# Performance work log

Hardware: AMD Instinct MI355X
Metric: run time of the kernel (lower is better)

Reference implementation:

```python
import jax, jax.numpy as jnp
import numpy as np

N_NODES = 100000


def _gcn_conv(x, W, b, row, col, norm, n):
    # PyG GCNConv: h = x @ W, then symmetric-normalized scatter-add, then bias
    h = x @ W                          # [N, out]
    msg = h[col] * norm[:, None]       # gather at source nodes, scale per-edge
    out = jax.ops.segment_sum(msg, row, num_segments=n)  # scatter-add to dest
    return out + b


def setup_inputs() -> dict:
    key = jax.random.key(0)
    k1, k2, k3, k4, k5, k6 = jax.random.split(key, 6)
    F_in, H, C = 128, 128, 64
    E = 1600000
    x = jax.random.normal(k1, (N_NODES, F_in), dtype=jnp.float32)
    edge_index = jax.random.randint(k2, (2, E), 0, N_NODES, dtype=jnp.int64)
    s1 = 1.0 / np.sqrt(F_in)
    s2 = 1.0 / np.sqrt(H)
    W1 = jax.random.uniform(k3, (F_in, H), jnp.float32, -s1, s1)
    b1 = jax.random.uniform(k4, (H,), jnp.float32, -s1, s1)
    W2 = jax.random.uniform(k5, (H, C), jnp.float32, -s2, s2)
    b2 = jax.random.uniform(k6, (C,), jnp.float32, -s2, s2)
    return {"x": x, "edge_index": edge_index, "W1": W1, "b1": b1, "W2": W2, "b2": b2}


def reference(x, edge_index, W1, b1, W2, b2):
    n = x.shape[0]
    # add self-loops (GCNConv default)
    loops = jnp.arange(n, dtype=edge_index.dtype)
    row = jnp.concatenate([edge_index[0], loops])  # destination
    col = jnp.concatenate([edge_index[1], loops])  # source
    # symmetric normalization deg^{-1/2}[row] * deg^{-1/2}[col]
    deg = jax.ops.segment_sum(jnp.ones_like(row, dtype=x.dtype), row, num_segments=n)
    dinv = jnp.where(deg > 0, jax.lax.rsqrt(deg), 0.0)
    norm = dinv[row] * dinv[col]       # [E+N]
    h = jax.nn.relu(_gcn_conv(x, W1, b1, row, col, norm, n))
    # dropout is identity in eval mode
    out = _gcn_conv(h, W2, b2, row, col, norm, n)
    return jax.nn.log_softmax(out, axis=1)
```

## Files before the change

kernel.cpp:

```cpp
#include <hip/hip_runtime.h>
#include <hip/hip_fp16.h>
#include <cstdint>
#include <cstddef>

#define TPB 256
#define CAP 64
#define FWSHIFT 9
#define FWROWS 512
#define CAPB 96
#define DEC_ITERS 32


using half8 = __attribute__((ext_vector_type(8))) _Float16;
using f32x4 = __attribute__((ext_vector_type(4))) float;
using i32x4 = __attribute__((ext_vector_type(4))) int;

struct GemmSm {
    _Float16 Wl[32 * 64 * 8];
    _Float16 Of[4][16 * 136];
};
struct FillSm { int cur[FWROWS]; };
union MegaSm { GemmSm g; FillSm f; };

__global__ __launch_bounds__(256)
void k_setup(const void* __restrict__ ei, int E, int N,
             const float* __restrict__ W2, _Float16* __restrict__ wf2,
             int* __restrict__ bpack, int* __restrict__ bcnt,
             int nDec, int nFW) {
    const int b = blockIdx.x;
    const int tid = threadIdx.x;

    if (b < 8) {
        int i = b * TPB + tid;
        int k  = i >> 4;
        int n0 = (i & 15) * 4;
        float4 w = ((const float4*)W2)[i];
        int ct = n0 >> 4, kb = k >> 5;
        int lane0 = ((k >> 3) & 3) * 16 + (n0 & 15);
        int j = k & 7;
        int base = ((ct * 4 + kb) * 64 + lane0) * 8 + j;
        wf2[base]      = (_Float16)w.x;
        wf2[base + 8]  = (_Float16)w.y;
        wf2[base + 16] = (_Float16)w.z;
        wf2[base + 24] = (_Float16)w.w;
    } else {
        __shared__ int cur[256];
        __shared__ int bad;
        const int dblk = b - 8;
        if (tid == 0) bad = 0;
        for (int f = tid; f < nFW; f += TPB) cur[f] = 0;
        __syncthreads();
        {
            long long v = ((const long long*)ei)[tid];
            if (v < 0 || v >= (long long)N) bad = 1;
        }
        __syncthreads();
        const int is64 = !bad;
        const int base = dblk * (TPB * DEC_ITERS);
        const long long* e64 = (const long long*)ei;
        const int* e32 = (const int*)ei;

        for (int it = 0; it < DEC_ITERS; it += 4) {
            int d[4], s[4]; bool val[4];
#pragma unroll
            for (int k = 0; k < 4; ++k) {
                int e = base + (it + k) * TPB + tid;
                val[k] = e < E;
                if (val[k]) {
                    if (is64) { d[k] = (int)e64[e]; s[k] = (int)e64[(long long)E + e]; }
                    else      { d[k] = e32[e];      s[k] = e32[E + e]; }
                }
            }
#pragma unroll
            for (int k = 0; k < 4; ++k) {
                if (val[k]) {
                    int fw  = d[k] >> FWSHIFT;
                    int pos = atomicAdd(&cur[fw], 1);
                    if (pos < CAPB)
                        bpack[((size_t)fw * nDec + dblk) * CAPB + pos] =
                            ((d[k] & (FWROWS - 1)) << 17) | s[k];
                }
            }
        }
        __syncthreads();
        for (int f = tid; f < nFW; f += TPB) {
            int c = cur[f];
            bcnt[(size_t)f * nDec + dblk] = c > CAPB ? CAPB : c;
        }
    }
}

__global__ __launch_bounds__(256)
void k_mega(const int* __restrict__ bpack, const int* __restrict__ bcnt,
            int nDec, int N,
            int* __restrict__ cnt, float* __restrict__ dinv,
            int* __restrict__ slots,
            const float* __restrict__ x, const float* __restrict__ W1,
            __half* __restrict__ xw1, int nFW, int nGemm) {
    __shared__ __align__(16) MegaSm sm;
    const int tid = threadIdx.x;

    if ((int)blockIdx.x < nFW) {
        const int fw = blockIdx.x;
        const int lo = fw << FWSHIFT;
        for (int i = tid; i < FWROWS; i += TPB) sm.f.cur[i] = 0;
        __syncthreads();

        for (int s = tid; s < nDec; s += TPB) {
            const int c = bcnt[(size_t)fw * nDec + s];
            const int* bp = bpack + ((size_t)fw * nDec + s) * CAPB;
            int j = 0;
            for (; j + 3 < c; j += 4) {
                i32x4 u = __builtin_nontemporal_load((const i32x4*)(bp + j));
                int dl0 = u[0] >> 17, s0 = u[0] & 0x1FFFF;
                int dl1 = u[1] >> 17, s1 = u[1] & 0x1FFFF;
                int dl2 = u[2] >> 17, s2 = u[2] & 0x1FFFF;
                int dl3 = u[3] >> 17, s3 = u[3] & 0x1FFFF;
                int q0 = atomicAdd(&sm.f.cur[dl0], 1);
                int q1 = atomicAdd(&sm.f.cur[dl1], 1);
                int q2 = atomicAdd(&sm.f.cur[dl2], 1);
                int q3 = atomicAdd(&sm.f.cur[dl3], 1);
                if (q0 < CAP) slots[(size_t)(lo + dl0) * CAP + q0] = s0;
                if (q1 < CAP) slots[(size_t)(lo + dl1) * CAP + q1] = s1;
                if (q2 < CAP) slots[(size_t)(lo + dl2) * CAP + q2] = s2;
                if (q3 < CAP) slots[(size_t)(lo + dl3) * CAP + q3] = s3;
            }
            for (; j < c; ++j) {
                int v = __builtin_nontemporal_load(bp + j);
                int dl = v >> 17, sv = v & 0x1FFFF;
                int pos = atomicAdd(&sm.f.cur[dl], 1);
                if (pos < CAP) slots[(size_t)(lo + dl) * CAP + pos] = sv;
            }
        }
        __syncthreads();
        for (int i = tid; i < FWROWS; i += TPB) {
            int node = lo + i;
            if (node < N) {
                int cc = sm.f.cur[i];
                cnt[node]  = cc;
                dinv[node] = rsqrtf((float)cc + 1.0f);
            }
        }
    } else {
        const int gb = (int)blockIdx.x - nFW;
        for (int i = tid; i < 4096; i += TPB) {
            float4 w = ((const float4*)W1)[i];
            int k  = i >> 5;
            int n0 = (i & 31) * 4;
            int ct = n0 >> 4, kb = k >> 5;
            int lane0 = ((k >> 3) & 3) * 16 + (n0 & 15);
            int j = k & 7;
            int bs = ((ct * 4 + kb) * 64 + lane0) * 8 + j;
            sm.g.Wl[bs]      = (_Float16)w.x;
            sm.g.Wl[bs + 8]  = (_Float16)w.y;
            sm.g.Wl[bs + 16] = (_Float16)w.z;
            sm.g.Wl[bs + 24] = (_Float16)w.w;
        }
        __syncthreads();
        const half8* wl = (const half8*)sm.g.Wl;
        const int wave = tid >> 6, lane = tid & 63;
        const int m = lane & 15, quad = lane >> 4;
        const int nRowTiles = (N + 15) >> 4;

        for (int rt = gb * 4 + wave; rt < nRowTiles; rt += nGemm * 4) {
            const int row0 = rt * 16;
            const int arow = row0 + m;
            const bool rvalid = arow < N;
            const float* xrow = x + (size_t)(rvalid ? arow : 0) * 128;

            f32x4 acc[8];
#pragma unroll
            for (int ct = 0; ct < 8; ++ct) acc[ct] = (f32x4){0.f, 0.f, 0.f, 0.f};

#pragma unroll
            for (int kb = 0; kb < 4; ++kb) {
                const float4* ap = (const float4*)(xrow + kb * 32 + quad * 8);
                float4 a0 = ap[0], a1 = ap[1];
                half8 a;
                a[0] = (_Float16)a0.x; a[1] = (_Float16)a0.y;
                a[2] = (_Float16)a0.z; a[3] = (_Float16)a0.w;
                a[4] = (_Float16)a1.x; a[5] = (_Float16)a1.y;
                a[6] = (_Float16)a1.z; a[7] = (_Float16)a1.w;
#pragma unroll
                for (int ct = 0; ct < 8; ++ct) {
                    half8 bfr = wl[(ct * 4 + kb) * 64 + lane];
                    acc[ct] = __builtin_amdgcn_mfma_f32_16x16x32_f16(a, bfr, acc[ct], 0, 0, 0);
                }
            }

            _Float16* myO = &sm.g.Of[wave][0];
#pragma unroll
            for (int ct = 0; ct < 8; ++ct)
#pragma unroll
                for (int r = 0; r < 4; ++r)
                    myO[(quad * 4 + r) * 136 + ct * 16 + m] = (_Float16)acc[ct][r];
            int vr = N - row0; if (vr > 16) vr = 16;
            float4* dst = (float4*)(xw1 + (size_t)row0 * 128);
            for (int i = lane; i < vr * 16; i += 64) {
                int r = i >> 4, q = i & 15;
                dst[r * 16 + q] = *(const float4*)&myO[r * 136 + q * 8];
            }
        }
    }
}

__global__ __launch_bounds__(256)
void k_g1g2(const __half* __restrict__ xw1, const int* __restrict__ cnt,
            const float* __restrict__ dinv,
            const int* __restrict__ slots, const float* __restrict__ bias,
            const half8* __restrict__ wf2, __half* __restrict__ xw2, int N) {
    __shared__ __align__(16) _Float16 Ht[16 * 136];
    __shared__ __align__(16) _Float16 Of[16 * 72];
    __shared__ float dv16[16];

    const int row0 = blockIdx.x * 16;
    const int local = threadIdx.x >> 4;
    const int lane16 = threadIdx.x & 15;
    const int node = row0 + local;

    {
        union { __half2 h2[4]; float4 f; } u;
        float dvn = 0.f;
        if (node < N) {
            int cn = cnt[node];
            int len = cn > CAP ? CAP : cn;
            dvn = dinv[node];
            const int* sl = slots + (size_t)node * CAP;
            float acc[8];
            {
                float4 raw = *(const float4*)(xw1 + (size_t)node * 128 + lane16 * 8);
                const __half2* hp = (const __half2*)&raw;
#pragma unroll
                for (int k = 0; k < 4; ++k) {
                    float2 f = __half22float2(hp[k]);
                    acc[2 * k] = dvn * f.x; acc[2 * k + 1] = dvn * f.y;
                }
            }
            int j = 0;
            for (; j + 3 < len; j += 4) {
                i32x4 cc = __builtin_nontemporal_load((const i32x4*)(sl + j));
                float dv0 = dinv[cc[0]];
                float dv1 = dinv[cc[1]];
                float dv2 = dinv[cc[2]];
                float dv3 = dinv[cc[3]];
                float4 raw0 = *(const float4*)(xw1 + (size_t)cc[0] * 128 + lane16 * 8);
                float4 raw1 = *(const float4*)(xw1 + (size_t)cc[1] * 128 + lane16 * 8);
                float4 raw2 = *(const float4*)(xw1 + (size_t)cc[2] * 128 + lane16 * 8);
                float4 raw3 = *(const float4*)(xw1 + (size_t)cc[3] * 128 + lane16 * 8);
                const __half2* h0 = (const __half2*)&raw0;
                const __half2* h1 = (const __half2*)&raw1;
                const __half2* h2 = (const __half2*)&raw2;
                const __half2* h3 = (const __half2*)&raw3;
#pragma unroll
                for (int k = 0; k < 4; ++k) {
                    float2 f0 = __half22float2(h0[k]);
                    float2 f1 = __half22float2(h1[k]);
                    float2 f2 = __half22float2(h2[k]);
                    float2 f3 = __half22float2(h3[k]);
                    acc[2 * k]     = fmaf(dv0, f0.x, fmaf(dv1, f1.x,
                                     fmaf(dv2, f2.x, fmaf(dv3, f3.x, acc[2 * k]))));
                    acc[2 * k + 1] = fmaf(dv0, f0.y, fmaf(dv1, f1.y,
                                     fmaf(dv2, f2.y, fmaf(dv3, f3.y, acc[2 * k + 1]))));
                }
            }
            for (; j < len; ++j) {
                int c = __builtin_nontemporal_load(sl + j);
                float dv = dinv[c];
                float4 raw = *(const float4*)(xw1 + (size_t)c * 128 + lane16 * 8);
                const __half2* hp = (const __half2*)&raw;
#pragma unroll
                for (int k = 0; k < 4; ++k) {
                    float2 f = __half22float2(hp[k]);
                    acc[2 * k]     = fmaf(dv, f.x, acc[2 * k]);
                    acc[2 * k + 1] = fmaf(dv, f.y, acc[2 * k + 1]);
                }
            }
            float4 b01 = ((const float4*)bias)[lane16 * 2];
            float4 b23 = ((const float4*)bias)[lane16 * 2 + 1];
            float v[8];
            v[0] = b01.x + dvn * acc[0]; v[1] = b01.y + dvn * acc[1];
            v[2] = b01.z + dvn * acc[2]; v[3] = b01.w + dvn * acc[3];
            v[4] = b23.x + dvn * acc[4]; v[5] = b23.y + dvn * acc[5];
            v[6] = b23.z + dvn * acc[6]; v[7] = b23.w + dvn * acc[7];
#pragma unroll
            for (int k = 0; k < 4; ++k)
                u.h2[k] = __floats2half2_rn(fmaxf(v[2 * k], 0.f), fmaxf(v[2 * k + 1], 0.f));
        } else {
            u.f = make_float4(0.f, 0.f, 0.f, 0.f);
        }
        if (lane16 == 0) dv16[local] = dvn;
        *(float4*)(Ht + local * 136 + lane16 * 8) = u.f;
    }
    __syncthreads();

    {
        const int wave = threadIdx.x >> 6, lane = threadIdx.x & 63;
        const int m = lane & 15, quad = lane >> 4;
        f32x4 acc = (f32x4){0.f, 0.f, 0.f, 0.f};
#pragma unroll
        for (int kb = 0; kb < 4; ++kb) {
            half8 a = *(const half8*)(Ht + m * 136 + kb * 32 + quad * 8);
            half8 b = wf2[(wave * 4 + kb) * 64 + lane];
            acc = __builtin_amdgcn_mfma_f32_16x16x32_f16(a, b, acc, 0, 0, 0);
        }
#pragma unroll
        for (int r = 0; r < 4; ++r)
            Of[(quad * 4 + r) * 72 + wave * 16 + m] =
                (_Float16)(acc[r] * dv16[quad * 4 + r]);
    }
    __syncthreads();
    {
        int vr = N - row0; if (vr > 16) vr = 16;
        float4* dst = (float4*)(xw2 + (size_t)row0 * 64);
        for (int i = threadIdx.x; i < vr * 8; i += TPB) {
            int r = i >> 3, q = i & 7;
            dst[r * 8 + q] = *(const float4*)&Of[r * 72 + q * 8];
        }
    }
}

__global__ void k_gather2_lsm(const __half* __restrict__ xws, const int* __restrict__ cnt,
                              const float* __restrict__ dinv,
                              const int* __restrict__ slots,
                              const float* __restrict__ bias, float* __restrict__ out, int N) {
    long long t = (long long)blockIdx.x * TPB + threadIdx.x;
    int node = (int)(t >> 3);
    int lane = (int)(t & 7);
    if (node >= N) return;
    int cn = cnt[node];
    int len = cn > CAP ? CAP : cn;
    float dvn = dinv[node];
    const int* sl = slots + (size_t)node * CAP;
    float a[8];
    {
        float4 raw = *(const float4*)(xws + (size_t)node * 64 + lane * 8);
        const __half2* hp = (const __half2*)&raw;
#pragma unroll
        for (int k = 0; k < 4; ++k) {
            float2 f = __half22float2(hp[k]);
            a[2 * k] = f.x; a[2 * k + 1] = f.y;
        }
    }
    int j = 0;
    for (; j + 3 < len; j += 4) {
        i32x4 cc = __builtin_nontemporal_load((const i32x4*)(sl + j));
        float4 r0 = *(const float4*)(xws + (size_t)cc[0] * 64 + lane * 8);
        float4 r1 = *(const float4*)(xws + (size_t)cc[1] * 64 + lane * 8);
        float4 r2 = *(const float4*)(xws + (size_t)cc[2] * 64 + lane * 8);
        float4 r3 = *(const float4*)(xws + (size_t)cc[3] * 64 + lane * 8);
        const __half2* h0 = (const __half2*)&r0;
        const __half2* h1 = (const __half2*)&r1;
        const __half2* h2 = (const __half2*)&r2;
        const __half2* h3 = (const __half2*)&r3;
#pragma unroll
        for (int k = 0; k < 4; ++k) {
            float2 f0 = __half22float2(h0[k]);
            float2 f1 = __half22float2(h1[k]);
            float2 f2 = __half22float2(h2[k]);
            float2 f3 = __half22float2(h3[k]);
            a[2 * k]     += (f0.x + f1.x) + (f2.x + f3.x);
            a[2 * k + 1] += (f0.y + f1.y) + (f2.y + f3.y);
        }
    }
    for (; j < len; ++j) {
        int c = __builtin_nontemporal_load(sl + j);
        float4 raw = *(const float4*)(xws + (size_t)c * 64 + lane * 8);
        const __half2* hp = (const __half2*)&raw;
#pragma unroll
        for (int k = 0; k < 4; ++k) {
            float2 f = __half22float2(hp[k]);
            a[2 * k] += f.x; a[2 * k + 1] += f.y;
        }
    }
    float4 b01 = ((const float4*)bias)[lane * 2];
    float4 b23 = ((const float4*)bias)[lane * 2 + 1];
    float v[8];
    v[0] = b01.x + dvn * a[0]; v[1] = b01.y + dvn * a[1];
    v[2] = b01.z + dvn * a[2]; v[3] = b01.w + dvn * a[3];
    v[4] = b23.x + dvn * a[4]; v[5] = b23.y + dvn * a[5];
    v[6] = b23.z + dvn * a[6]; v[7] = b23.w + dvn * a[7];

    float m = v[0];
#pragma unroll
    for (int k = 1; k < 8; ++k) m = fmaxf(m, v[k]);
#pragma unroll
    for (int off = 1; off < 8; off <<= 1) m = fmaxf(m, __shfl_xor(m, off));
    float s = 0.f;
#pragma unroll
    for (int k = 0; k < 8; ++k) s += expf(v[k] - m);
#pragma unroll
    for (int off = 1; off < 8; off <<= 1) s += __shfl_xor(s, off);
    float ls = m + logf(s);
    float4 o0 = make_float4(v[0] - ls, v[1] - ls, v[2] - ls, v[3] - ls);
    float4 o1 = make_float4(v[4] - ls, v[5] - ls, v[6] - ls, v[7] - ls);
    ((float4*)(out + (size_t)node * 64))[lane * 2]     = o0;
    ((float4*)(out + (size_t)node * 64))[lane * 2 + 1] = o1;
}

extern "C" void kernel_launch(void* const* d_in, const int* in_sizes, int n_in,
                              void* d_out, int out_size, void* d_ws, size_t ws_size,
                              hipStream_t stream) {
    const float* x  = (const float*)d_in[0];
    const void*  ei = d_in[1];
    const float* W1 = (const float*)d_in[2];
    const float* b1 = (const float*)d_in[3];
    const float* W2 = (const float*)d_in[4];
    const float* b2 = (const float*)d_in[5];
    float* out = (float*)d_out;

    const int N = in_sizes[0] / 128;
    const int E = in_sizes[1] / 2;

    const int nFW  = (N + FWROWS - 1) >> FWSHIFT;
    const int nDec = (E + TPB * DEC_ITERS - 1) / (TPB * DEC_ITERS);
    const int nGemm = 512;

    char* base = (char*)d_ws;
    size_t off = 0;
    auto alloc = [&](size_t bytes) { char* p = base + off; off = (off + bytes + 255) & ~(size_t)255; return p; };
    int*      cnt    = (int*)alloc((size_t)N * sizeof(int));
    float*    dinv   = (float*)alloc((size_t)N * sizeof(float));
    _Float16* wf2    = (_Float16*)alloc(128 * 64 * sizeof(_Float16));
    int*      bcnt   = (int*)alloc((size_t)nFW * nDec * sizeof(int));
    int*      bpack  = (int*)alloc((size_t)nFW * nDec * CAPB * sizeof(int));
    int*      slots  = (int*)alloc((size_t)N * CAP * sizeof(int));
    __half*   xw1    = (__half*)alloc((size_t)N * 128 * sizeof(__half));
    __half*   xw2    = (__half*)alloc((size_t)N * 64 * sizeof(__half));
    (void)ws_size;

    const int nodeTiles = (N + 15) / 16;

    k_setup<<<8 + nDec, TPB, 0, stream>>>(ei, E, N, W2, wf2, bpack, bcnt,
                                          nDec, nFW);

    k_mega<<<nFW + nGemm, TPB, 0, stream>>>(bpack, bcnt, nDec, N, cnt, dinv,
                                            slots, x, W1, xw1, nFW, nGemm);

    k_g1g2<<<nodeTiles, TPB, 0, stream>>>(xw1, cnt, dinv, slots, b1,
                                          (const half8*)wf2, xw2, N);

    {
        long long t = (long long)N * 8;
        k_gather2_lsm<<<(int)((t + TPB - 1) / TPB), TPB, 0, stream>>>(xw2, cnt, dinv, slots, b2, out, N);
    }
}
```

Measured before the change: 260.1 us.

## Stage edge bins in shared memory via prefix scan and write compactly

The edge-decode kernel now counts edges per destination window, runs a shared-memory prefix scan, and scatters the packed edges into a shared buffer. It then writes them contiguously per decode block with per-window base offsets and counts, replacing fixed CAPB-sized per-window slots. This drops the capacity-truncation path and replaces scattered global writes with coalesced ones, shrinking the bpack workspace. The consumer reads with scalar loads at unaligned offsets, and nontemporal loads are replaced by plain loads in all gather kernels. Costs are more syncs and register/LDS pressure in setup, and scalar rather than vector bin reads in k_mega.

Result: faster. 238.2 us (-8.4%).

```diff
diff --git a/kernel.cpp b/kernel.cpp
--- a/kernel.cpp
+++ b/kernel.cpp
@@ -7,13 +7,12 @@
 #define CAP 64
 #define FWSHIFT 9
 #define FWROWS 512
-#define CAPB 96
 #define DEC_ITERS 32
+#define DEC_EDGES (TPB * DEC_ITERS)
 
 
 using half8 = __attribute__((ext_vector_type(8))) _Float16;
 using f32x4 = __attribute__((ext_vector_type(4))) float;
-using i32x4 = __attribute__((ext_vector_type(4))) int;
 
 struct GemmSm {
     _Float16 Wl[32 * 64 * 8];
@@ -25,8 +24,13 @@
 __global__ __launch_bounds__(256)
 void k_setup(const void* __restrict__ ei, int E, int N,
              const float* __restrict__ W2, _Float16* __restrict__ wf2,
-             int* __restrict__ bpack, int* __restrict__ bcnt,
-             int nDec, int nFW) {
+             int* __restrict__ bpack, int* __restrict__ bbase,
+             int* __restrict__ bcnt, int nDec, int nFW) {
+    __shared__ int buf[DEC_EDGES];
+    __shared__ int lcnt[256];
+    __shared__ int lofs[256];
+    __shared__ int sc[256];
+    __shared__ int bad;
     const int b = blockIdx.x;
     const int tid = threadIdx.x;
 
@@ -43,56 +47,73 @@
         wf2[base + 8]  = (_Float16)w.y;
         wf2[base + 16] = (_Float16)w.z;
         wf2[base + 24] = (_Float16)w.w;
-    } else {
-        __shared__ int cur[256];
-        __shared__ int bad;
-        const int dblk = b - 8;
-        if (tid == 0) bad = 0;
-        for (int f = tid; f < nFW; f += TPB) cur[f] = 0;
+        return;
+    }
+
+    const int dblk = b - 8;
+    if (tid == 0) bad = 0;
+    lcnt[tid] = 0;
+    __syncthreads();
+    {
+        long long v = ((const long long*)ei)[tid];
+        if (v < 0 || v >= (long long)N) bad = 1;
+    }
+    __syncthreads();
+    const int is64 = !bad;
+    const int base = dblk * DEC_EDGES;
+    const long long* e64 = (const long long*)ei;
+    const int* e32 = (const int*)ei;
+
+    int pv[DEC_ITERS];
+    int pfw[DEC_ITERS];
+#pragma unroll
+    for (int k = 0; k < DEC_ITERS; ++k) {
+        int e = base + k * TPB + tid;
+        pfw[k] = -1;
+        pv[k] = 0;
+        if (e < E) {
+            int d, s;
+            if (is64) { d = (int)e64[e]; s = (int)e64[(long long)E + e]; }
+            else      { d = e32[e];      s = e32[E + e]; }
+            pfw[k] = d >> FWSHIFT;
+            pv[k]  = ((d & (FWROWS - 1)) << 17) | s;
+            atomicAdd(&lcnt[pfw[k]], 1);
+        }
+    }
+    __syncthreads();
+
+    int c = lcnt[tid];
+    sc[tid] = c;
+    __syncthreads();
+    for (int off = 1; off < 256; off <<= 1) {
+        int v = (tid >= off) ? sc[tid - off] : 0;
         __syncthreads();
-        {
-            long long v = ((const long long*)ei)[tid];
-            if (v < 0 || v >= (long long)N) bad = 1;
-        }
+        sc[tid] += v;
         __syncthreads();
-        const int is64 = !bad;
-        const int base = dblk * (TPB * DEC_ITERS);
-        const long long* e64 = (const long long*)ei;
-        const int* e32 = (const int*)ei;
-
-        for (int it = 0; it < DEC_ITERS; it += 4) {
-            int d[4], s[4]; bool val[4];
-#pragma unroll
-            for (int k = 0; k < 4; ++k) {
-                int e = base + (it + k) * TPB + tid;
-                val[k] = e < E;
-                if (val[k]) {
-                    if (is64) { d[k] = (int)e64[e]; s[k] = (int)e64[(long long)E + e]; }
-                    else      { d[k] = e32[e];      s[k] = e32[E + e]; }
-                }
-            }
-#pragma unroll
-            for (int k = 0; k < 4; ++k) {
-                if (val[k]) {
-                    int fw  = d[k] >> FWSHIFT;
-                    int pos = atomicAdd(&cur[fw], 1);
-                    if (pos < CAPB)
-                        bpack[((size_t)fw * nDec + dblk) * CAPB + pos] =
-                            ((d[k] & (FWROWS - 1)) << 17) | s[k];
-                }
-            }
-        }
-        __syncthreads();
-        for (int f = tid; f < nFW; f += TPB) {
-            int c = cur[f];
-            bcnt[(size_t)f * nDec + dblk] = c > CAPB ? CAPB : c;
-        }
+    }
+    lofs[tid] = sc[tid] - c;
+    __syncthreads();
+#pragma unroll
+    for (int k = 0; k < DEC_ITERS; ++k) {
+        if (pfw[k] >= 0) {
+            int pos = atomicAdd(&lofs[pfw[k]], 1);
+            buf[pos] = pv[k];
+        }
+    }
+    __syncthreads();
+
+    const int total = sc[255];
+    for (int i = tid; i < total; i += TPB)
+        bpack[(size_t)dblk * DEC_EDGES + i] = buf[i];
+    if (tid < nFW) {
+        bbase[(size_t)tid * nDec + dblk] = sc[tid] - c;
+        bcnt [(size_t)tid * nDec + dblk] = c;
     }
 }
 
 __global__ __launch_bounds__(256)
-void k_mega(const int* __restrict__ bpack, const int* __restrict__ bcnt,
-            int nDec, int N,
+void k_mega(const int* __restrict__ bpack, const int* __restrict__ bbase,
+            const int* __restrict__ bcnt, int nDec, int N,
             int* __restrict__ cnt, float* __restrict__ dinv,
             int* __restrict__ slots,
             const float* __restrict__ x, const float* __restrict__ W1,
@@ -107,15 +128,16 @@
         __syncthreads();
 
         for (int s = tid; s < nDec; s += TPB) {
-            const int c = bcnt[(size_t)fw * nDec + s];
-            const int* bp = bpack + ((size_t)fw * nDec + s) * CAPB;
+            const size_t seg = (size_t)fw * nDec + s;
+            const int c = bcnt[seg];
+            const int* bp = bpack + (size_t)s * DEC_EDGES + bbase[seg];
             int j = 0;
             for (; j + 3 < c; j += 4) {
-                i32x4 u = __builtin_nontemporal_load((const i32x4*)(bp + j));
-                int dl0 = u[0] >> 17, s0 = u[0] & 0x1FFFF;
-                int dl1 = u[1] >> 17, s1 = u[1] & 0x1FFFF;
-                int dl2 = u[2] >> 17, s2 = u[2] & 0x1FFFF;
-                int dl3 = u[3] >> 17, s3 = u[3] & 0x1FFFF;
+                int v0 = bp[j], v1 = bp[j + 1], v2 = bp[j + 2], v3 = bp[j + 3];
+                int dl0 = v0 >> 17, s0 = v0 & 0x1FFFF;
+                int dl1 = v1 >> 17, s1 = v1 & 0x1FFFF;
+                int dl2 = v2 >> 17, s2 = v2 & 0x1FFFF;
+                int dl3 = v3 >> 17, s3 = v3 & 0x1FFFF;
                 int q0 = atomicAdd(&sm.f.cur[dl0], 1);
                 int q1 = atomicAdd(&sm.f.cur[dl1], 1);
                 int q2 = atomicAdd(&sm.f.cur[dl2], 1);
@@ -126,7 +148,7 @@
                 if (q3 < CAP) slots[(size_t)(lo + dl3) * CAP + q3] = s3;
             }
             for (; j < c; ++j) {
-                int v = __builtin_nontemporal_load(bp + j);
+                int v = bp[j];
                 int dl = v >> 17, sv = v & 0x1FFFF;
                 int pos = atomicAdd(&sm.f.cur[dl], 1);
                 if (pos < CAP) slots[(size_t)(lo + dl) * CAP + pos] = sv;
@@ -238,15 +260,15 @@
             }
             int j = 0;
             for (; j + 3 < len; j += 4) {
-                i32x4 cc = __builtin_nontemporal_load((const i32x4*)(sl + j));
-                float dv0 = dinv[cc[0]];
-                float dv1 = dinv[cc[1]];
-                float dv2 = dinv[cc[2]];
-                float dv3 = dinv[cc[3]];
-                float4 raw0 = *(const float4*)(xw1 + (size_t)cc[0] * 128 + lane16 * 8);
-                float4 raw1 = *(const float4*)(xw1 + (size_t)cc[1] * 128 + lane16 * 8);
-                float4 raw2 = *(const float4*)(xw1 + (size_t)cc[2] * 128 + lane16 * 8);
-                float4 raw3 = *(const float4*)(xw1 + (size_t)cc[3] * 128 + lane16 * 8);
+                int4 cc = *(const int4*)(sl + j);
+                float dv0 = dinv[cc.x];
+                float dv1 = dinv[cc.y];
+                float dv2 = dinv[cc.z];
+                float dv3 = dinv[cc.w];
+                float4 raw0 = *(const float4*)(xw1 + (size_t)cc.x * 128 + lane16 * 8);
+                float4 raw1 = *(const float4*)(xw1 + (size_t)cc.y * 128 + lane16 * 8);
+                float4 raw2 = *(const float4*)(xw1 + (size_t)cc.z * 128 + lane16 * 8);
+                float4 raw3 = *(const float4*)(xw1 + (size_t)cc.w * 128 + lane16 * 8);
                 const __half2* h0 = (const __half2*)&raw0;
                 const __half2* h1 = (const __half2*)&raw1;
                 const __half2* h2 = (const __half2*)&raw2;
@@ -264,7 +286,7 @@
                 }
             }
             for (; j < len; ++j) {
-                int c = __builtin_nontemporal_load(sl + j);
+                int c = sl[j];
                 float dv = dinv[c];
                 float4 raw = *(const float4*)(xw1 + (size_t)c * 128 + lane16 * 8);
                 const __half2* hp = (const __half2*)&raw;
@@ -343,11 +365,11 @@
     }
     int j = 0;
     for (; j + 3 < len; j += 4) {
-        i32x4 cc = __builtin_nontemporal_load((const i32x4*)(sl + j));
-        float4 r0 = *(const float4*)(xws + (size_t)cc[0] * 64 + lane * 8);
-        float4 r1 = *(const float4*)(xws + (size_t)cc[1] * 64 + lane * 8);
-        float4 r2 = *(const float4*)(xws + (size_t)cc[2] * 64 + lane * 8);
-        float4 r3 = *(const float4*)(xws + (size_t)cc[3] * 64 + lane * 8);
+        int4 cc = *(const int4*)(sl + j);
+        float4 r0 = *(const float4*)(xws + (size_t)cc.x * 64 + lane * 8);
+        float4 r1 = *(const float4*)(xws + (size_t)cc.y * 64 + lane * 8);
+        float4 r2 = *(const float4*)(xws + (size_t)cc.z * 64 + lane * 8);
+        float4 r3 = *(const float4*)(xws + (size_t)cc.w * 64 + lane * 8);
         const __half2* h0 = (const __half2*)&r0;
         const __half2* h1 = (const __half2*)&r1;
         const __half2* h2 = (const __half2*)&r2;
@@ -363,7 +385,7 @@
         }
     }
     for (; j < len; ++j) {
-        int c = __builtin_nontemporal_load(sl + j);
+        int c = sl[j];
         float4 raw = *(const float4*)(xws + (size_t)c * 64 + lane * 8);
         const __half2* hp = (const __half2*)&raw;
 #pragma unroll
@@ -412,7 +434,7 @@
     const int E = in_sizes[1] / 2;
 
     const int nFW  = (N + FWROWS - 1) >> FWSHIFT;
-    const int nDec = (E + TPB * DEC_ITERS - 1) / (TPB * DEC_ITERS);
+    const int nDec = (E + DEC_EDGES - 1) / DEC_EDGES;
     const int nGemm = 512;
 
     char* base = (char*)d_ws;
@@ -421,8 +443,9 @@
     int*      cnt    = (int*)alloc((size_t)N * sizeof(int));
     float*    dinv   = (float*)alloc((size_t)N * sizeof(float));
     _Float16* wf2    = (_Float16*)alloc(128 * 64 * sizeof(_Float16));
+    int*      bbase  = (int*)alloc((size_t)nFW * nDec * sizeof(int));
     int*      bcnt   = (int*)alloc((size_t)nFW * nDec * sizeof(int));
-    int*      bpack  = (int*)alloc((size_t)nFW * nDec * CAPB * sizeof(int));
+    int*      bpack  = (int*)alloc((size_t)nDec * DEC_EDGES * sizeof(int));
     int*      slots  = (int*)alloc((size_t)N * CAP * sizeof(int));
     __half*   xw1    = (__half*)alloc((size_t)N * 128 * sizeof(__half));
     __half*   xw2    = (__half*)alloc((size_t)N * 64 * sizeof(__half));
@@ -430,11 +453,11 @@
 
     const int nodeTiles = (N + 15) / 16;
 
-    k_setup<<<8 + nDec, TPB, 0, stream>>>(ei, E, N, W2, wf2, bpack, bcnt,
-                                          nDec, nFW);
-
-    k_mega<<<nFW + nGemm, TPB, 0, stream>>>(bpack, bcnt, nDec, N, cnt, dinv,
-                                            slots, x, W1, xw1, nFW, nGemm);
+    k_setup<<<8 + nDec, TPB, 0, stream>>>(ei, E, N, W2, wf2, bpack, bbase,
+                                          bcnt, nDec, nFW);
+
+    k_mega<<<nFW + nGemm, TPB, 0, stream>>>(bpack, bbase, bcnt, nDec, N, cnt,
+                                            dinv, slots, x, W1, xw1, nFW, nGemm);
 
     k_g1g2<<<nodeTiles, TPB, 0, stream>>>(xw1, cnt, dinv, slots, b1,
                                           (const half8*)wf2, xw2, N);
```
